# Optimization experiments

Hardware: AMD Instinct MI355X
Metric: run time of the kernel (lower is better)

Reference implementation:

```python
import jax, jax.numpy as jnp
import numpy as np

EPS = 1e-6
NH, HD = 8, 16            # num_heads, head_dim (dim=128)
KSS, DILS, HPR = (3, 5), (1, 2), (6, 2)  # kernel sizes, dilations, heads per range (favor_small)


def gelu(t):
    return jax.nn.gelu(t, approximate=False)


def conv1x1(x, w, b):
    # x: (B,C,H,W), w: (O,C), b: (O,)
    return jnp.einsum('oc,bchw->bohw', w, x) + b[None, :, None, None]


def dwconv(x, w, b, dil=1):
    # depthwise conv, w: (C,1,k,k)
    k = w.shape[-1]
    p = (k // 2) * dil
    y = jax.lax.conv_general_dilated(
        x, w, window_strides=(1, 1), padding=[(p, p), (p, p)],
        rhs_dilation=(dil, dil), feature_group_count=x.shape[1],
        dimension_numbers=('NCHW', 'OIHW', 'NCHW'))
    return y + b[None, :, None, None]


def ln2d(x, w, b):
    # LayerNorm over channel dim of NCHW
    mu = x.mean(axis=1, keepdims=True)
    var = ((x - mu) ** 2).mean(axis=1, keepdims=True)
    return (x - mu) * jax.lax.rsqrt(var + EPS) * w[None, :, None, None] + b[None, :, None, None]


def unfold(x, ks, dil):
    # x: (B,h,d,H,W) -> (B,h,d,L,H,W) with L=ks*ks neighborhood (row-major, matches F.unfold)
    B, h, d, H, W = x.shape
    p = (ks // 2) * dil
    xp = jnp.pad(x, ((0, 0), (0, 0), (0, 0), (p, p), (p, p)))
    patches = [xp[..., i * dil:i * dil + H, j * dil:j * dil + W]
               for i in range(ks) for j in range(ks)]
    return jnp.stack(patches, axis=3)


def neighborhood_attn(x, qkv_ws, qkv_bs, proj_w, proj_b):
    B, C, H, W = x.shape
    scale = HD ** -0.5
    outs, hs = [], 0
    for i in range(2):
        qkv = conv1x1(x, qkv_ws[i], qkv_bs[i]).reshape(B, 3, NH, HD, H, W)
        he = hs + HPR[i]
        q, k, v = qkv[:, 0, hs:he], qkv[:, 1, hs:he], qkv[:, 2, hs:he]
        k_nb = unfold(k, KSS[i], DILS[i])  # (B,h,d,L,H,W)
        v_nb = unfold(v, KSS[i], DILS[i])
        logits = jnp.einsum('bhdxy,bhdlxy->bhlxy', q * scale, k_nb)
        attn = jax.nn.softmax(logits, axis=2)
        outs.append(jnp.einsum('bhlxy,bhdlxy->bhdxy', attn, v_nb))
        hs = he
    out = jnp.concatenate(outs, axis=1).reshape(B, C, H, W)
    return conv1x1(out, proj_w, proj_b)


def msconvstar(x, fc1_w, fc1_b, dw_ws, dw_bs, fc2_w, fc2_b):
    h = conv1x1(x, fc1_w, fc1_b)                  # (B,192,H,W)
    xs = jnp.split(h, [64, 128], axis=1)          # channels [64,64,64] for dw_sizes (1,3,5)
    ys = [dwconv(t, w, b) for t, w, b in zip(xs, dw_ws, dw_bs)]
    h = h + jnp.concatenate(ys, axis=1)
    x1, x2 = jnp.split(h, 2, axis=1)
    return conv1x1(gelu(x1) * x2, fc2_w, fc2_b)


def cascaded_sparse(x, dw0_w, dw0_b, dw1_w, dw1_b, pw_w, pw_b):
    x = gelu(dwconv(x, dw0_w, dw0_b, dil=1))
    x = gelu(dwconv(x, dw1_w, dw1_b, dil=2))
    return conv1x1(x, pw_w, pw_b)


def setup_inputs() -> dict:
    key = jax.random.key(0)
    ks = jax.random.split(key, 24)
    C, HID = 128, 192

    def p(k, shape, s=0.02):
        return jax.random.normal(k, shape, jnp.float32) * s

    d = {'x': jax.random.normal(ks[0], (4, C, 80, 80), jnp.float32)}
    for i in (1, 2, 3, 4):
        d[f'n{i}_w'] = jnp.ones((C,), jnp.float32)
        d[f'n{i}_b'] = jnp.zeros((C,), jnp.float32)
    d['qkv0_w'] = p(ks[1], (3 * C, C)); d['qkv0_b'] = jnp.zeros((3 * C,), jnp.float32)
    d['qkv1_w'] = p(ks[2], (3 * C, C)); d['qkv1_b'] = jnp.zeros((3 * C,), jnp.float32)
    d['ma_proj_w'] = p(ks[3], (C, C)); d['ma_proj_b'] = jnp.zeros((C,), jnp.float32)
    for pre, k0 in (('m1', 4), ('m2', 10)):
        d[f'{pre}_fc1_w'] = p(ks[k0], (HID, C)); d[f'{pre}_fc1_b'] = jnp.zeros((HID,), jnp.float32)
        for j, dk in enumerate((1, 3, 5)):
            d[f'{pre}_dw{j}_w'] = p(ks[k0 + 1 + j], (64, 1, dk, dk))
            d[f'{pre}_dw{j}_b'] = jnp.zeros((64,), jnp.float32)
        d[f'{pre}_fc2_w'] = p(ks[k0 + 4], (C, HID // 2)); d[f'{pre}_fc2_b'] = jnp.zeros((C,), jnp.float32)
    d['sma_dw0_w'] = p(ks[16], (C, 1, 3, 3)); d['sma_dw0_b'] = jnp.zeros((C,), jnp.float32)
    d['sma_dw1_w'] = p(ks[17], (C, 1, 3, 3)); d['sma_dw1_b'] = jnp.zeros((C,), jnp.float32)
    d['sma_pw_w'] = p(ks[18], (C, C)); d['sma_pw_b'] = jnp.zeros((C,), jnp.float32)
    return d


def reference(x, n1_w, n1_b, n2_w, n2_b, n3_w, n3_b, n4_w, n4_b,
              qkv0_w, qkv0_b, qkv1_w, qkv1_b, ma_proj_w, ma_proj_b,
              m1_fc1_w, m1_fc1_b, m1_dw0_w, m1_dw0_b, m1_dw1_w, m1_dw1_b,
              m1_dw2_w, m1_dw2_b, m1_fc2_w, m1_fc2_b,
              sma_dw0_w, sma_dw0_b, sma_dw1_w, sma_dw1_b, sma_pw_w, sma_pw_b,
              m2_fc1_w, m2_fc1_b, m2_dw0_w, m2_dw0_b, m2_dw1_w, m2_dw1_b,
              m2_dw2_w, m2_dw2_b, m2_fc2_w, m2_fc2_b):
    x = x + neighborhood_attn(ln2d(x, n1_w, n1_b), (qkv0_w, qkv1_w), (qkv0_b, qkv1_b), ma_proj_w, ma_proj_b)
    x = x + msconvstar(ln2d(x, n2_w, n2_b), m1_fc1_w, m1_fc1_b,
                       (m1_dw0_w, m1_dw1_w, m1_dw2_w), (m1_dw0_b, m1_dw1_b, m1_dw2_b), m1_fc2_w, m1_fc2_b)
    x = x + cascaded_sparse(ln2d(x, n3_w, n3_b), sma_dw0_w, sma_dw0_b, sma_dw1_w, sma_dw1_b, sma_pw_w, sma_pw_b)
    x = x + msconvstar(ln2d(x, n4_w, n4_b), m2_fc1_w, m2_fc1_b,
                       (m2_dw0_w, m2_dw1_w, m2_dw2_w), (m2_dw0_b, m2_dw1_b, m2_dw2_b), m2_fc2_w, m2_fc2_b)
    return x
```

## Files before the change

kernel.cpp:

```cpp
#include <hip/hip_runtime.h>
#include <math.h>

#define Hn 80
#define Wn 80
#define HWn 6400

typedef unsigned short u16;
typedef __attribute__((ext_vector_type(8))) short s16x8;
typedef __attribute__((ext_vector_type(4))) float f32x4;

__device__ __forceinline__ float gelu_exact(float v) {
  return 0.5f * v * (1.f + erff(v * 0.70710678118654752f));
}
__device__ __forceinline__ u16 f2bf(float x) {
  unsigned u = __float_as_uint(x);
  return (u16)((u + 0x7fffu + ((u >> 16) & 1u)) >> 16);
}
typedef __attribute__((address_space(1))) const unsigned int* gptr_t;
typedef __attribute__((address_space(3))) unsigned int* lptr_t;
__device__ __forceinline__ void gld16(const void* g, void* l) {
  __builtin_amdgcn_global_load_lds((gptr_t)g, (lptr_t)l, 16, 0, 0);
}
__device__ __forceinline__ void ld16h(const u16* p, float* f) {
  uint4 a = *(const uint4*)p;
  uint4 c = *(const uint4*)(p + 8);
  unsigned w[8] = {a.x, a.y, a.z, a.w, c.x, c.y, c.z, c.w};
  #pragma unroll
  for (int j = 0; j < 8; ++j) {
    f[2 * j]     = __uint_as_float(w[j] << 16);
    f[2 * j + 1] = __uint_as_float(w[j] & 0xffff0000u);
  }
}

__global__ __launch_bounds__(256) void wprep_k(
    const float* __restrict__ q0w, const float* __restrict__ q0b,
    const float* __restrict__ q1w, const float* __restrict__ q1b,
    const float* __restrict__ projw, const float* __restrict__ f1w_1,
    const float* __restrict__ f2w_1, const float* __restrict__ pww,
    const float* __restrict__ f1w_2, const float* __restrict__ f2w_2,
    u16* Wq, float* Bq, u16* Wp, u16* Wf1a, u16* Wf2a, u16* Wpw, u16* Wf1b, u16* Wf2b) {
  int idx = blockIdx.x * 256 + threadIdx.x;
  if (idx < 49152) {
    int r = idx >> 7, ic = idx & 127;
    int sel = r >> 7, c = r & 127;
    const float* src = ((c >> 4) < 6 ? q0w : q1w);
    Wq[idx] = f2bf(src[(size_t)(sel * 128 + c) * 128 + ic]);
    return;
  }
  idx -= 49152;
  if (idx < 16384) { Wp[idx] = f2bf(projw[idx]); return; }
  idx -= 16384;
  if (idx < 24576) { Wf1a[idx] = f2bf(f1w_1[idx]); return; }
  idx -= 24576;
  if (idx < 16384) { int oc = idx >> 7, ic = idx & 127;
    Wf2a[idx] = ic < 96 ? f2bf(f2w_1[oc * 96 + ic]) : (u16)0; return; }
  idx -= 16384;
  if (idx < 16384) { Wpw[idx] = f2bf(pww[idx]); return; }
  idx -= 16384;
  if (idx < 24576) { Wf1b[idx] = f2bf(f1w_2[idx]); return; }
  idx -= 24576;
  if (idx < 16384) { int oc = idx >> 7, ic = idx & 127;
    Wf2b[idx] = ic < 96 ? f2bf(f2w_2[oc * 96 + ic]) : (u16)0; return; }
  idx -= 16384;
  if (idx < 384) {
    int sel = idx >> 7, c = idx & 127;
    Bq[idx] = ((c >> 4) < 6 ? q0b : q1b)[sel * 128 + c];
  }
}

template<int TMODE>
__global__ __launch_bounds__(256) void ln_k(const float* __restrict__ in,
    const float* __restrict__ gw, const float* __restrict__ gb, void* __restrict__ outv) {
  __shared__ float sS[4][64];
  __shared__ float sQ[4][64];
  __shared__ unsigned sT[64 * 64];
  const int b = blockIdx.y;
  const int p0 = blockIdx.x * 64;
  const int tid = threadIdx.x;
  const int px = tid & 63;
  const int cg = tid >> 6;
  const float* ip = in + (size_t)b * 128 * HWn + p0 + px;
  float s = 0.f, q = 0.f;
  #pragma unroll 8
  for (int c = cg * 32; c < cg * 32 + 32; ++c) { float v = ip[(size_t)c * HWn]; s += v; q += v * v; }
  sS[cg][px] = s; sQ[cg][px] = q;
  __syncthreads();
  float S = sS[0][px] + sS[1][px] + sS[2][px] + sS[3][px];
  float Q = sQ[0][px] + sQ[1][px] + sQ[2][px] + sQ[3][px];
  float mu = S * (1.f / 128.f);
  float rs = rsqrtf(Q * (1.f / 128.f) - mu * mu + 1e-6f);
  #pragma unroll
  for (int j = 0; j < 16; ++j) {
    int c0 = cg * 32 + 2 * j;
    float v0 = ip[(size_t)c0 * HWn];
    float v1 = ip[(size_t)(c0 + 1) * HWn];
    v0 = (v0 - mu) * rs * gw[c0] + gb[c0];
    v1 = (v1 - mu) * rs * gw[c0 + 1] + gb[c0 + 1];
    int wc = cg * 16 + j;
    sT[px * 64 + (wc ^ (px & 31))] = (unsigned)f2bf(v0) | ((unsigned)f2bf(v1) << 16);
  }
  __syncthreads();
  u16* ob = (u16*)outv + ((size_t)b * HWn + p0) * 128;
  #pragma unroll
  for (int it = 0; it < 4; ++it) {
    int opx = it * 16 + (tid >> 4);
    int chunk = tid & 15;
    unsigned w[4];
    #pragma unroll
    for (int j = 0; j < 4; ++j)
      w[j] = sT[opx * 64 + ((chunk * 4 + j) ^ (opx & 31))];
    *(uint4*)(ob + (size_t)opx * 128 + chunk * 8) = make_uint4(w[0], w[1], w[2], w[3]);
  }
}

__global__ __launch_bounds__(256) void lnstats_k(const float* __restrict__ in,
                                                 float2* __restrict__ st) {
  __shared__ float sS[4][64];
  __shared__ float sQ[4][64];
  const int b = blockIdx.y;
  const int p0 = blockIdx.x * 64;
  const int tid = threadIdx.x;
  const int px = tid & 63;
  const int cg = tid >> 6;
  const float* ip = in + (size_t)b * 128 * HWn + p0 + px;
  float s = 0.f, q = 0.f;
  #pragma unroll 8
  for (int c = cg * 32; c < cg * 32 + 32; ++c) { float v = ip[(size_t)c * HWn]; s += v; q += v * v; }
  sS[cg][px] = s; sQ[cg][px] = q;
  __syncthreads();
  if (cg == 0) {
    float S = sS[0][px] + sS[1][px] + sS[2][px] + sS[3][px];
    float Q = sQ[0][px] + sQ[1][px] + sQ[2][px] + sQ[3][px];
    float mu = S * (1.f / 128.f);
    float rs = rsqrtf(Q * (1.f / 128.f) - mu * mu + 1e-6f);
    st[(size_t)b * HWn + p0 + px] = make_float2(mu, rs);
  }
}

__device__ __forceinline__ s16x8 ldfrag(const u16* s, int row, int gk) {
  return *(const s16x8*)(s + row * 128 + ((gk ^ (row & 7)) << 3));
}

template<int ORIENT, int RES, int SPLITQ>
__global__ __launch_bounds__(256) void gemm_k(
    const u16* __restrict__ Xg, const u16* __restrict__ Wg,
    const float* __restrict__ bias, const float* __restrict__ resid,
    float* __restrict__ outF, u16* __restrict__ outH, int OCT) {
  __shared__ u16 sX[128 * 128];
  __shared__ u16 sW[64 * 128];
  const int tid = threadIdx.x, lane = tid & 63, wv = tid >> 6;
  const int b = blockIdx.y;
  const int px0 = blockIdx.x * 128;
  const int oc0 = blockIdx.z * 64;
  const u16* xb = Xg + ((size_t)b * HWn + px0) * 128;
  const u16* wb = Wg + (size_t)oc0 * 128;
  #pragma unroll
  for (int i = 0; i < 8; ++i) {
    int o16 = (wv * 8 + i) * 64 + lane;
    int r = o16 >> 4, g = o16 & 15;
    gld16(xb + (size_t)r * 128 + ((g ^ (r & 7)) << 3), (char*)sX + (size_t)(wv * 8 + i) * 1024);
  }
  #pragma unroll
  for (int i = 0; i < 4; ++i) {
    int o16 = (wv * 4 + i) * 64 + lane;
    int r = o16 >> 4, g = o16 & 15;
    gld16(wb + (size_t)r * 128 + ((g ^ (r & 7)) << 3), (char*)sW + (size_t)(wv * 4 + i) * 1024);
  }
  __syncthreads();
  const int l15 = lane & 15, l4 = lane >> 4;
  if (ORIENT == 0) {
    f32x4 acc[4][2] = {};
    #pragma unroll
    for (int ks = 0; ks < 4; ++ks) {
      int gk = ks * 4 + l4;
      s16x8 a[4], bb[2];
      #pragma unroll
      for (int mi = 0; mi < 4; ++mi) a[mi] = ldfrag(sW, mi * 16 + l15, gk);
      #pragma unroll
      for (int ni = 0; ni < 2; ++ni) bb[ni] = ldfrag(sX, wv * 32 + ni * 16 + l15, gk);
      #pragma unroll
      for (int mi = 0; mi < 4; ++mi)
        #pragma unroll
        for (int ni = 0; ni < 2; ++ni)
          acc[mi][ni] = __builtin_amdgcn_mfma_f32_16x16x32_bf16(a[mi], bb[ni], acc[mi][ni], 0, 0, 0);
    }
    #pragma unroll
    for (int mi = 0; mi < 4; ++mi) {
      #pragma unroll
      for (int rr = 0; rr < 4; ++rr) {
        int oc = oc0 + mi * 16 + l4 * 4 + rr;
        float bv = bias[oc];
        #pragma unroll
        for (int ni = 0; ni < 2; ++ni) {
          size_t idx = ((size_t)b * OCT + oc) * HWn + px0 + wv * 32 + ni * 16 + l15;
          float v = acc[mi][ni][rr] + bv;
          if (RES) v += resid[idx];
          outF[idx] = v;
        }
      }
    }
  } else {
    f32x4 acc[2][4] = {};
    #pragma unroll
    for (int ks = 0; ks < 4; ++ks) {
      int gk = ks * 4 + l4;
      s16x8 a[2], bb[4];
      #pragma unroll
      for (int mi = 0; mi < 2; ++mi) a[mi] = ldfrag(sX, wv * 32 + mi * 16 + l15, gk);
      #pragma unroll
      for (int ni = 0; ni < 4; ++ni) bb[ni] = ldfrag(sW, ni * 16 + l15, gk);
      #pragma unroll
      for (int mi = 0; mi < 2; ++mi)
        #pragma unroll
        for (int ni = 0; ni < 4; ++ni)
          acc[mi][ni] = __builtin_amdgcn_mfma_f32_16x16x32_bf16(a[mi], bb[ni], acc[mi][ni], 0, 0, 0);
    }
    #pragma unroll
    for (int ni = 0; ni < 4; ++ni) {
      int oc = oc0 + ni * 16 + l15;
      float bv = bias[oc];
      #pragma unroll
      for (int mi = 0; mi < 2; ++mi) {
        #pragma unroll
        for (int rr = 0; rr < 4; ++rr) {
          int px = px0 + wv * 32 + mi * 16 + l4 * 4 + rr;
          float v = acc[mi][ni][rr] + bv;
          u16 hv = f2bf(v);
          if (SPLITQ) {
            int sel = oc >> 7, c = oc & 127;
            int head = c >> 4, d = c & 15;
            outH[((((size_t)sel * 8 + head) * 4 + b) * HWn + px) * 16 + d] = hv;
          } else {
            outH[((size_t)b * HWn + px) * (size_t)OCT + oc] = hv;
          }
        }
      }
    }
  }
}

template<int KS, int DIL>
__device__ __forceinline__ void natt_body(const u16* __restrict__ qkv,
                                          u16* __restrict__ out, int b, int h, int p) {
  const int y = p / Wn, x = p - (p / Wn) * Wn;
  const u16* Qb = qkv + (((size_t)h * 4 + b) * HWn) * 16;
  const u16* Kb = qkv + ((((size_t)8 + h) * 4 + b) * HWn) * 16;
  const u16* Vb = qkv + ((((size_t)16 + h) * 4 + b) * HWn) * 16;
  float qv[16];
  ld16h(Qb + (size_t)p * 16, qv);
  #pragma unroll
  for (int d = 0; d < 16; ++d) qv[d] *= 0.25f;
  constexpr int L = KS * KS;
  float lg[L];
  #pragma unroll
  for (int i = 0; i < KS; ++i) {
    #pragma unroll
    for (int j = 0; j < KS; ++j) {
      int yy = y + (i - KS / 2) * DIL;
      int xx = x + (j - KS / 2) * DIL;
      float a = 0.f;
      if (yy >= 0 && yy < Hn && xx >= 0 && xx < Wn) {
        float kv[16];
        ld16h(Kb + (size_t)(yy * Wn + xx) * 16, kv);
        #pragma unroll
        for (int d = 0; d < 16; ++d) a = fmaf(qv[d], kv[d], a);
      }
      lg[i * KS + j] = a;
    }
  }
  float mx = lg[0];
  #pragma unroll
  for (int l = 1; l < L; ++l) mx = fmaxf(mx, lg[l]);
  float sum = 0.f;
  #pragma unroll
  for (int l = 0; l < L; ++l) { float e = __expf(lg[l] - mx); lg[l] = e; sum += e; }
  float inv = 1.f / sum;
  float acc[16];
  #pragma unroll
  for (int d = 0; d < 16; ++d) acc[d] = 0.f;
  #pragma unroll
  for (int i = 0; i < KS; ++i) {
    #pragma unroll
    for (int j = 0; j < KS; ++j) {
      int yy = y + (i - KS / 2) * DIL;
      int xx = x + (j - KS / 2) * DIL;
      if (yy >= 0 && yy < Hn && xx >= 0 && xx < Wn) {
        float vv[16];
        ld16h(Vb + (size_t)(yy * Wn + xx) * 16, vv);
        float wl = lg[i * KS + j] * inv;
        #pragma unroll
        for (int d = 0; d < 16; ++d) acc[d] = fmaf(wl, vv[d], acc[d]);
      }
    }
  }
  unsigned wst[8];
  #pragma unroll
  for (int j = 0; j < 8; ++j)
    wst[j] = (unsigned)f2bf(acc[2 * j]) | ((unsigned)f2bf(acc[2 * j + 1]) << 16);
  u16* op = out + ((size_t)b * HWn + p) * 128 + h * 16;
  *(uint4*)op = make_uint4(wst[0], wst[1], wst[2], wst[3]);
  *(uint4*)(op + 8) = make_uint4(wst[4], wst[5], wst[6], wst[7]);
}

__global__ __launch_bounds__(256) void natt_k(const u16* __restrict__ qkv,
                                              u16* __restrict__ out) {
  const int b = blockIdx.y, h = blockIdx.z;
  const int p = blockIdx.x * 256 + threadIdx.x;
  if (h < 6) natt_body<3, 1>(qkv, out, b, h, p);
  else       natt_body<5, 2>(qkv, out, b, h, p);
}

template<int R>
__device__ __forceinline__ void stage_plane(const float* __restrict__ plane,
                                            float* __restrict__ s,
                                            int ty0, int tx0, int tid) {
  constexpr int D = 16 + 2 * R, PD = D + 1;
  #pragma unroll
  for (int i = tid; i < D * D; i += 256) {
    int ey = i / D, ex = i - ey * D;
    int gy = ty0 - R + ey, gx = tx0 - R + ex;
    float v = 0.f;
    if (gy >= 0 && gy < Hn && gx >= 0 && gx < Wn) v = plane[gy * Wn + gx];
    s[ey * PD + ex] = v;
  }
}

template<int R>
__device__ __forceinline__ float dw_from_lds(const float* __restrict__ s, int ly, int lx,
                                             const float* __restrict__ w, float bv) {
  constexpr int PD = 16 + 2 * R + 1;
  float center = s[(ly + R) * PD + (lx + R)];
  float acc = bv;
  #pragma unroll
  for (int i = 0; i < 2 * R + 1; ++i)
    #pragma unroll
    for (int j = 0; j < 2 * R + 1; ++j)
      acc = fmaf(w[i * (2 * R + 1) + j], s[(ly + i) * PD + (lx + j)], acc);
  return center + acc;
}

template<int R1, int R2>
__device__ __forceinline__ void star_pairs(const float* __restrict__ hb,
    const float* __restrict__ w0, const float* __restrict__ b0,
    const float* __restrict__ w1, const float* __restrict__ b1,
    const float* __restrict__ w2, const float* __restrict__ b2,
    float* __restrict__ s1_0, float* __restrict__ s1_1,
    float* __restrict__ s2_0, float* __restrict__ s2_1,
    int z, int ty0, int tx0, int tid, int ly, int lx, unsigned* __restrict__ res) {
  if (R1 > 0) stage_plane<R1>(hb + (size_t)(z * 8) * HWn, s1_0, ty0, tx0, tid);
  stage_plane<R2>(hb + (size_t)(z * 8 + 96) * HWn, s2_0, ty0, tx0, tid);
  __syncthreads();
  #pragma unroll 1
  for (int pi = 0; pi < 8; ++pi) {
    int c1 = z * 8 + pi;
    int c2 = c1 + 96;
    float* s1c = (pi & 1) ? s1_1 : s1_0;
    float* s2c = (pi & 1) ? s2_1 : s2_0;
    if (pi < 7) {
      float* s1n = (pi & 1) ? s1_0 : s1_1;
      float* s2n = (pi & 1) ? s2_0 : s2_1;
      if (R1 > 0) stage_plane<R1>(hb + (size_t)(c1 + 1) * HWn, s1n, ty0, tx0, tid);
      stage_plane<R2>(hb + (size_t)(c2 + 1) * HWn, s2n, ty0, tx0, tid);
    }
    float h1;
    if constexpr (R1 == 0) {
      float cen = hb[(size_t)c1 * HWn + (ty0 + ly) * Wn + tx0 + lx];
      h1 = cen + fmaf(cen, w0[c1], b0[c1]);
    } else {
      h1 = dw_from_lds<R1>(s1c, ly, lx, w1 + (c1 - 64) * 9, b1[c1 - 64]);
    }
    float h2;
    if constexpr (R2 == 1) {
      h2 = dw_from_lds<1>(s2c, ly, lx, w1 + (c2 - 64) * 9, b1[c2 - 64]);
    } else {
      h2 = dw_from_lds<2>(s2c, ly, lx, w2 + (c2 - 128) * 25, b2[c2 - 128]);
    }
    u16 gv = f2bf(gelu_exact(h1) * h2);
    if (pi & 1) res[pi >> 1] |= ((unsigned)gv) << 16;
    else        res[pi >> 1] = (unsigned)gv;
    __syncthreads();
  }
}

__global__ __launch_bounds__(256) void star_k(const float* __restrict__ hbuf,
    const float* __restrict__ w0, const float* __restrict__ b0,
    const float* __restrict__ w1, const float* __restrict__ b1,
    const float* __restrict__ w2, const float* __restrict__ b2,
    u16* __restrict__ g) {
  __shared__ float s1_0[18 * 19];
  __shared__ float s1_1[18 * 19];
  __shared__ float s2_0[20 * 21];
  __shared__ float s2_1[20 * 21];
  const int b = blockIdx.y, z = blockIdx.z;
  const int tile = blockIdx.x;
  const int ty0 = (tile / 5) * 16, tx0 = (tile % 5) * 16;
  const int tid = threadIdx.x;
  const int ly = tid >> 4, lx = tid & 15;
  const float* hb = hbuf + (size_t)b * 192 * HWn;
  unsigned res[4];
  if (z < 4)      star_pairs<0, 1>(hb, w0, b0, w1, b1, w2, b2, s1_0, s1_1, s2_0, s2_1, z, ty0, tx0, tid, ly, lx, res);
  else if (z < 8) star_pairs<0, 2>(hb, w0, b0, w1, b1, w2, b2, s1_0, s1_1, s2_0, s2_1, z, ty0, tx0, tid, ly, lx, res);
  else            star_pairs<1, 2>(hb, w0, b0, w1, b1, w2, b2, s1_0, s1_1, s2_0, s2_1, z, ty0, tx0, tid, ly, lx, res);
  const int px = (ty0 + ly) * Wn + tx0 + lx;
  *(uint4*)(g + ((size_t)b * HWn + px) * 128 + z * 8) = make_uint4(res[0], res[1], res[2], res[3]);
  if (z < 4)
    *(uint4*)(g + ((size_t)b * HWn + px) * 128 + 96 + z * 8) = make_uint4(0, 0, 0, 0);
}

__global__ __launch_bounds__(256) void dwgf_k(const float* __restrict__ xin,
    const float2* __restrict__ st,
    const float* __restrict__ gw, const float* __restrict__ gb,
    const float* __restrict__ w1, const float* __restrict__ b1,
    const float* __restrict__ w2, const float* __restrict__ b2,
    u16* __restrict__ out) {
  __shared__ float sA[22 * 23];
  __shared__ float sB[20 * 21];
  __shared__ float sMu[22 * 22];
  __shared__ float sRs[22 * 22];
  const int b = blockIdx.y, z = blockIdx.z;
  const int tile = blockIdx.x;
  const int ty0 = (tile / 5) * 16, tx0 = (tile % 5) * 16;
  const int tid = threadIdx.x;
  const int ly = tid >> 4, lx = tid & 15;
  #pragma unroll
  for (int i = tid; i < 22 * 22; i += 256) {
    int ey = i / 22, ex = i - ey * 22;
    int gy = ty0 - 3 + ey, gx = tx0 - 3 + ex;
    float2 s = make_float2(0.f, 0.f);
    if (gy >= 0 && gy < Hn && gx >= 0 && gx < Wn) s = st[(size_t)b * HWn + gy * Wn + gx];
    sMu[i] = s.x; sRs[i] = s.y;
  }
  const float* xb = xin + (size_t)b * 128 * HWn;
  unsigned res[4];
  #pragma unroll 1
  for (int ci = 0; ci < 8; ++ci) {
    int c = z * 8 + ci;
    const float* xp = xb + (size_t)c * HWn;
    float gwc = gw[c], gbc = gb[c];
    __syncthreads();
    #pragma unroll
    for (int i = tid; i < 22 * 22; i += 256) {
      int ey = i / 22, ex = i - ey * 22;
      int gy = ty0 - 3 + ey, gx = tx0 - 3 + ex;
      float v = 0.f;
      if (gy >= 0 && gy < Hn && gx >= 0 && gx < Wn)
        v = (xp[gy * Wn + gx] - sMu[i]) * sRs[i] * gwc + gbc;
      sA[ey * 23 + ex] = v;
    }
    __syncthreads();
    #pragma unroll
    for (int j = tid; j < 20 * 20; j += 256) {
      int by = j / 20, bx = j - by * 20;
      int gy = ty0 - 2 + by, gx = tx0 - 2 + bx;
      float r = 0.f;
      if (gy >= 0 && gy < Hn && gx >= 0 && gx < Wn) {
        float acc = b1[c];
        #pragma unroll
        for (int di = 0; di < 3; ++di)
          #pragma unroll
          for (int dj = 0; dj < 3; ++dj)
            acc = fmaf(w1[c * 9 + di * 3 + dj], sA[(by + di) * 23 + (bx + dj)], acc);
        r = gelu_exact(acc);
      }
      sB[by * 21 + bx] = r;
    }
    __syncthreads();
    float acc = b2[c];
    #pragma unroll
    for (int di = 0; di < 3; ++di)
      #pragma unroll
      for (int dj = 0; dj < 3; ++dj)
        acc = fmaf(w2[c * 9 + di * 3 + dj], sB[(ly + 2 * di) * 21 + (lx + 2 * dj)], acc);
    float r = gelu_exact(acc);
    u16 gv = f2bf(r);
    if (ci & 1) res[ci >> 1] |= ((unsigned)gv) << 16;
    else        res[ci >> 1] = (unsigned)gv;
  }
  const int px = (ty0 + ly) * Wn + tx0 + lx;
  *(uint4*)(out + ((size_t)b * HWn + px) * 128 + z * 8) = make_uint4(res[0], res[1], res[2], res[3]);
}

extern "C" void kernel_launch(void* const* d_in, const int* in_sizes, int n_in,
                              void* d_out, int out_size, void* d_ws, size_t ws_size,
                              hipStream_t stream) {
  (void)in_sizes; (void)n_in; (void)out_size; (void)ws_size;
  const float* x      = (const float*)d_in[0];
  const float* n1w    = (const float*)d_in[1];
  const float* n1b    = (const float*)d_in[2];
  const float* n2w    = (const float*)d_in[3];
  const float* n2b    = (const float*)d_in[4];
  const float* n3w    = (const float*)d_in[5];
  const float* n3b    = (const float*)d_in[6];
  const float* n4w    = (const float*)d_in[7];
  const float* n4b    = (const float*)d_in[8];
  const float* qkv0w  = (const float*)d_in[9];
  const float* qkv0b  = (const float*)d_in[10];
  const float* qkv1w  = (const float*)d_in[11];
  const float* qkv1b  = (const float*)d_in[12];
  const float* projw  = (const float*)d_in[13];
  const float* projb  = (const float*)d_in[14];
  const float* m1fc1w = (const float*)d_in[15];
  const float* m1fc1b = (const float*)d_in[16];
  const float* m1dw0w = (const float*)d_in[17];
  const float* m1dw0b = (const float*)d_in[18];
  const float* m1dw1w = (const float*)d_in[19];
  const float* m1dw1b = (const float*)d_in[20];
  const float* m1dw2w = (const float*)d_in[21];
  const float* m1dw2b = (const float*)d_in[22];
  const float* m1fc2w = (const float*)d_in[23];
  const float* m1fc2b = (const float*)d_in[24];
  const float* smadw0w = (const float*)d_in[25];
  const float* smadw0b = (const float*)d_in[26];
  const float* smadw1w = (const float*)d_in[27];
  const float* smadw1b = (const float*)d_in[28];
  const float* smapww  = (const float*)d_in[29];
  const float* smapwb  = (const float*)d_in[30];
  const float* m2fc1w = (const float*)d_in[31];
  const float* m2fc1b = (const float*)d_in[32];
  const float* m2dw0w = (const float*)d_in[33];
  const float* m2dw0b = (const float*)d_in[34];
  const float* m2dw1w = (const float*)d_in[35];
  const float* m2dw1b = (const float*)d_in[36];
  const float* m2dw2w = (const float*)d_in[37];
  const float* m2dw2b = (const float*)d_in[38];
  const float* m2fc2w = (const float*)d_in[39];
  const float* m2fc2b = (const float*)d_in[40];

  float* out = (float*)d_out;
  char* wsb = (char*)d_ws;
  u16*  QKV = (u16*)(wsb + 0);
  float* Hb = (float*)(wsb + 0);
  u16*  LNo = (u16*)(wsb + 19660800);
  u16*  ATT = (u16*)(wsb + 26214400);
  u16*  T2  = (u16*)(wsb + 32768000);
  char* wp = wsb + 39321600;
  u16* Wq    = (u16*)wp;  wp += 98304;
  u16* Wproj = (u16*)wp;  wp += 32768;
  u16* Wf1a  = (u16*)wp;  wp += 49152;
  u16* Wf2a  = (u16*)wp;  wp += 32768;
  u16* Wpw   = (u16*)wp;  wp += 32768;
  u16* Wf1b  = (u16*)wp;  wp += 49152;
  u16* Wf2b  = (u16*)wp;  wp += 32768;
  float* Bq  = (float*)wp; wp += 2048;
  float2* Stats = (float2*)wp;

  dim3 blk(256);
  wprep_k<<<642, blk, 0, stream>>>(qkv0w, qkv0b, qkv1w, qkv1b, projw, m1fc1w, m1fc2w,
                                   smapww, m2fc1w, m2fc2w,
                                   Wq, Bq, Wproj, Wf1a, Wf2a, Wpw, Wf1b, Wf2b);

  ln_k<1><<<dim3(100, 4), blk, 0, stream>>>(x, n1w, n1b, LNo);
  gemm_k<1, 0, 1><<<dim3(50, 4, 6), blk, 0, stream>>>(LNo, Wq, Bq, nullptr, nullptr, QKV, 384);
  natt_k<<<dim3(25, 4, 8), blk, 0, stream>>>(QKV, ATT);
  gemm_k<0, 1, 0><<<dim3(50, 4, 2), blk, 0, stream>>>(ATT, Wproj, projb, x, out, nullptr, 128);

  ln_k<1><<<dim3(100, 4), blk, 0, stream>>>(out, n2w, n2b, LNo);
  gemm_k<0, 0, 0><<<dim3(50, 4, 3), blk, 0, stream>>>(LNo, Wf1a, m1fc1b, nullptr, Hb, nullptr, 192);
  star_k<<<dim3(25, 4, 12), blk, 0, stream>>>(Hb, m1dw0w, m1dw0b, m1dw1w, m1dw1b, m1dw2w, m1dw2b, ATT);
  gemm_k<0, 1, 0><<<dim3(50, 4, 2), blk, 0, stream>>>(ATT, Wf2a, m1fc2b, out, out, nullptr, 128);

  lnstats_k<<<dim3(100, 4), blk, 0, stream>>>(out, Stats);
  dwgf_k<<<dim3(25, 4, 16), blk, 0, stream>>>(out, Stats, n3w, n3b,
                                              smadw0w, smadw0b, smadw1w, smadw1b, T2);
  gemm_k<0, 1, 0><<<dim3(50, 4, 2), blk, 0, stream>>>(T2, Wpw, smapwb, out, out, nullptr, 128);

  ln_k<1><<<dim3(100, 4), blk, 0, stream>>>(out, n4w, n4b, LNo);
  gemm_k<0, 0, 0><<<dim3(50, 4, 3), blk, 0, stream>>>(LNo, Wf1b, m2fc1b, nullptr, Hb, nullptr, 192);
  star_k<<<dim3(25, 4, 12), blk, 0, stream>>>(Hb, m2dw0w, m2dw0b, m2dw1w, m2dw1b, m2dw2w, m2dw2b, ATT);
  gemm_k<0, 1, 0><<<dim3(50, 4, 2), blk, 0, stream>>>(ATT, Wf2b, m2fc2b, out, out, nullptr, 128);
}
```

Measured before the change: 169.0 us.

## Tile neighborhood attention with LDS halos and store fc1 output as bf16

The neighborhood attention kernel is split into two templated launches (3x3 dil1 and 5x5 dil2). Each block now stages a 16x16 tile of K and V plus its halo into shared memory, which removes per-neighbor bounds checks and redundant global loads. Separately, the fc1 GEMM writes its intermediate in bf16 instead of fp32, and the star depthwise kernel reads bf16. This halves that buffer's traffic but adds rounding to an intermediate that was previously kept in fp32.

```diff
diff --git a/kernel.cpp b/kernel.cpp
--- a/kernel.cpp
+++ b/kernel.cpp
@@ -15,6 +15,9 @@
 __device__ __forceinline__ u16 f2bf(float x) {
   unsigned u = __float_as_uint(x);
   return (u16)((u + 0x7fffu + ((u >> 16) & 1u)) >> 16);
+}
+__device__ __forceinline__ float bf2f(u16 h) {
+  return __uint_as_float(((unsigned)h) << 16);
 }
 typedef __attribute__((address_space(1))) const unsigned int* gptr_t;
 typedef __attribute__((address_space(3))) unsigned int* lptr_t;
@@ -68,9 +71,8 @@
   }
 }
 
-template<int TMODE>
 __global__ __launch_bounds__(256) void ln_k(const float* __restrict__ in,
-    const float* __restrict__ gw, const float* __restrict__ gb, void* __restrict__ outv) {
+    const float* __restrict__ gw, const float* __restrict__ gb, u16* __restrict__ outv) {
   __shared__ float sS[4][64];
   __shared__ float sQ[4][64];
   __shared__ unsigned sT[64 * 64];
@@ -100,7 +102,7 @@
     sT[px * 64 + (wc ^ (px & 31))] = (unsigned)f2bf(v0) | ((unsigned)f2bf(v1) << 16);
   }
   __syncthreads();
-  u16* ob = (u16*)outv + ((size_t)b * HWn + p0) * 128;
+  u16* ob = outv + ((size_t)b * HWn + p0) * 128;
   #pragma unroll
   for (int it = 0; it < 4; ++it) {
     int opx = it * 16 + (tid >> 4);
@@ -141,7 +143,7 @@
   return *(const s16x8*)(s + row * 128 + ((gk ^ (row & 7)) << 3));
 }
 
-template<int ORIENT, int RES, int SPLITQ>
+template<int ORIENT, int RES, int SPLITQ, int H16>
 __global__ __launch_bounds__(256) void gemm_k(
     const u16* __restrict__ Xg, const u16* __restrict__ Wg,
     const float* __restrict__ bias, const float* __restrict__ resid,
@@ -194,8 +196,12 @@
         for (int ni = 0; ni < 2; ++ni) {
           size_t idx = ((size_t)b * OCT + oc) * HWn + px0 + wv * 32 + ni * 16 + l15;
           float v = acc[mi][ni][rr] + bv;
-          if (RES) v += resid[idx];
-          outF[idx] = v;
+          if (H16) {
+            outH[idx] = f2bf(v);
+          } else {
+            if (RES) v += resid[idx];
+            outF[idx] = v;
+          }
         }
       }
     }
@@ -240,31 +246,50 @@
 }
 
 template<int KS, int DIL>
-__device__ __forceinline__ void natt_body(const u16* __restrict__ qkv,
-                                          u16* __restrict__ out, int b, int h, int p) {
-  const int y = p / Wn, x = p - (p / Wn) * Wn;
+__global__ __launch_bounds__(256) void natt_k(const u16* __restrict__ qkv,
+                                              u16* __restrict__ out, int h0) {
+  constexpr int HALO = DIL * (KS / 2);
+  constexpr int D = 16 + 2 * HALO;
+  __shared__ u16 sK[D * D * 16];
+  __shared__ u16 sV[D * D * 16];
+  const int b = blockIdx.y, h = h0 + blockIdx.z;
+  const int tile = blockIdx.x;
+  const int ty0 = (tile / 5) * 16, tx0 = (tile % 5) * 16;
+  const int tid = threadIdx.x;
+  const int ly = tid >> 4, lx = tid & 15;
   const u16* Qb = qkv + (((size_t)h * 4 + b) * HWn) * 16;
   const u16* Kb = qkv + ((((size_t)8 + h) * 4 + b) * HWn) * 16;
   const u16* Vb = qkv + ((((size_t)16 + h) * 4 + b) * HWn) * 16;
+  for (int i = tid; i < D * D * 2; i += 256) {
+    int pxi = i >> 1, half = i & 1;
+    int ey = pxi / D, ex = pxi - ey * D;
+    int gy = ty0 - HALO + ey, gx = tx0 - HALO + ex;
+    uint4 kv = make_uint4(0, 0, 0, 0), vv = make_uint4(0, 0, 0, 0);
+    if (gy >= 0 && gy < Hn && gx >= 0 && gx < Wn) {
+      size_t off = (size_t)(gy * Wn + gx) * 16 + half * 8;
+      kv = *(const uint4*)(Kb + off);
+      vv = *(const uint4*)(Vb + off);
+    }
+    *(uint4*)(sK + pxi * 16 + half * 8) = kv;
+    *(uint4*)(sV + pxi * 16 + half * 8) = vv;
+  }
+  const int p = (ty0 + ly) * Wn + tx0 + lx;
   float qv[16];
   ld16h(Qb + (size_t)p * 16, qv);
   #pragma unroll
   for (int d = 0; d < 16; ++d) qv[d] *= 0.25f;
+  __syncthreads();
   constexpr int L = KS * KS;
   float lg[L];
   #pragma unroll
   for (int i = 0; i < KS; ++i) {
     #pragma unroll
     for (int j = 0; j < KS; ++j) {
-      int yy = y + (i - KS / 2) * DIL;
-      int xx = x + (j - KS / 2) * DIL;
+      float kvv[16];
+      ld16h(sK + (size_t)((ly + i * DIL) * D + lx + j * DIL) * 16, kvv);
       float a = 0.f;
-      if (yy >= 0 && yy < Hn && xx >= 0 && xx < Wn) {
-        float kv[16];
-        ld16h(Kb + (size_t)(yy * Wn + xx) * 16, kv);
-        #pragma unroll
-        for (int d = 0; d < 16; ++d) a = fmaf(qv[d], kv[d], a);
-      }
+      #pragma unroll
+      for (int d = 0; d < 16; ++d) a = fmaf(qv[d], kvv[d], a);
       lg[i * KS + j] = a;
     }
   }
@@ -282,15 +307,11 @@
   for (int i = 0; i < KS; ++i) {
     #pragma unroll
     for (int j = 0; j < KS; ++j) {
-      int yy = y + (i - KS / 2) * DIL;
-      int xx = x + (j - KS / 2) * DIL;
-      if (yy >= 0 && yy < Hn && xx >= 0 && xx < Wn) {
-        float vv[16];
-        ld16h(Vb + (size_t)(yy * Wn + xx) * 16, vv);
-        float wl = lg[i * KS + j] * inv;
-        #pragma unroll
-        for (int d = 0; d < 16; ++d) acc[d] = fmaf(wl, vv[d], acc[d]);
-      }
+      float vv[16];
+      ld16h(sV + (size_t)((ly + i * DIL) * D + lx + j * DIL) * 16, vv);
+      float wl = lg[i * KS + j] * inv;
+      #pragma unroll
+      for (int d = 0; d < 16; ++d) acc[d] = fmaf(wl, vv[d], acc[d]);
     }
   }
   unsigned wst[8];
@@ -302,16 +323,8 @@
   *(uint4*)(op + 8) = make_uint4(wst[4], wst[5], wst[6], wst[7]);
 }
 
-__global__ __launch_bounds__(256) void natt_k(const u16* __restrict__ qkv,
-                                              u16* __restrict__ out) {
-  const int b = blockIdx.y, h = blockIdx.z;
-  const int p = blockIdx.x * 256 + threadIdx.x;
-  if (h < 6) natt_body<3, 1>(qkv, out, b, h, p);
-  else       natt_body<5, 2>(qkv, out, b, h, p);
-}
-
 template<int R>
-__device__ __forceinline__ void stage_plane(const float* __restrict__ plane,
+__device__ __forceinline__ void stage_plane(const u16* __restrict__ plane,
                                             float* __restrict__ s,
                                             int ty0, int tx0, int tid) {
   constexpr int D = 16 + 2 * R, PD = D + 1;
@@ -320,7 +333,7 @@
     int ey = i / D, ex = i - ey * D;
     int gy = ty0 - R + ey, gx = tx0 - R + ex;
     float v = 0.f;
-    if (gy >= 0 && gy < Hn && gx >= 0 && gx < Wn) v = plane[gy * Wn + gx];
+    if (gy >= 0 && gy < Hn && gx >= 0 && gx < Wn) v = bf2f(plane[gy * Wn + gx]);
     s[ey * PD + ex] = v;
   }
 }
@@ -340,7 +353,7 @@
 }
 
 template<int R1, int R2>
-__device__ __forceinline__ void star_pairs(const float* __restrict__ hb,
+__device__ __forceinline__ void star_pairs(const u16* __restrict__ hb,
     const float* __restrict__ w0, const float* __restrict__ b0,
     const float* __restrict__ w1, const float* __restrict__ b1,
     const float* __restrict__ w2, const float* __restrict__ b2,
@@ -364,7 +377,7 @@
     }
     float h1;
     if constexpr (R1 == 0) {
-      float cen = hb[(size_t)c1 * HWn + (ty0 + ly) * Wn + tx0 + lx];
+      float cen = bf2f(hb[(size_t)c1 * HWn + (ty0 + ly) * Wn + tx0 + lx]);
       h1 = cen + fmaf(cen, w0[c1], b0[c1]);
     } else {
       h1 = dw_from_lds<R1>(s1c, ly, lx, w1 + (c1 - 64) * 9, b1[c1 - 64]);
@@ -382,7 +395,7 @@
   }
 }
 
-__global__ __launch_bounds__(256) void star_k(const float* __restrict__ hbuf,
+__global__ __launch_bounds__(256) void star_k(const u16* __restrict__ hbuf,
     const float* __restrict__ w0, const float* __restrict__ b0,
     const float* __restrict__ w1, const float* __restrict__ b1,
     const float* __restrict__ w2, const float* __restrict__ b2,
@@ -396,7 +409,7 @@
   const int ty0 = (tile / 5) * 16, tx0 = (tile % 5) * 16;
   const int tid = threadIdx.x;
   const int ly = tid >> 4, lx = tid & 15;
-  const float* hb = hbuf + (size_t)b * 192 * HWn;
+  const u16* hb = hbuf + (size_t)b * 192 * HWn;
   unsigned res[4];
   if (z < 4)      star_pairs<0, 1>(hb, w0, b0, w1, b1, w2, b2, s1_0, s1_1, s2_0, s2_1, z, ty0, tx0, tid, ly, lx, res);
   else if (z < 8) star_pairs<0, 2>(hb, w0, b0, w1, b1, w2, b2, s1_0, s1_1, s2_0, s2_1, z, ty0, tx0, tid, ly, lx, res);
@@ -529,7 +542,7 @@
   float* out = (float*)d_out;
   char* wsb = (char*)d_ws;
   u16*  QKV = (u16*)(wsb + 0);
-  float* Hb = (float*)(wsb + 0);
+  u16*  Hb16 = (u16*)(wsb + 0);
   u16*  LNo = (u16*)(wsb + 19660800);
   u16*  ATT = (u16*)(wsb + 26214400);
   u16*  T2  = (u16*)(wsb + 32768000);
@@ -549,23 +562,24 @@
                                    smapww, m2fc1w, m2fc2w,
                                    Wq, Bq, Wproj, Wf1a, Wf2a, Wpw, Wf1b, Wf2b);
 
-  ln_k<1><<<dim3(100, 4), blk, 0, stream>>>(x, n1w, n1b, LNo);
-  gemm_k<1, 0, 1><<<dim3(50, 4, 6), blk, 0, stream>>>(LNo, Wq, Bq, nullptr, nullptr, QKV, 384);
-  natt_k<<<dim3(25, 4, 8), blk, 0, stream>>>(QKV, ATT);
-  gemm_k<0, 1, 0><<<dim3(50, 4, 2), blk, 0, stream>>>(ATT, Wproj, projb, x, out, nullptr, 128);
-
-  ln_k<1><<<dim3(100, 4), blk, 0, stream>>>(out, n2w, n2b, LNo);
-  gemm_k<0, 0, 0><<<dim3(50, 4, 3), blk, 0, stream>>>(LNo, Wf1a, m1fc1b, nullptr, Hb, nullptr, 192);
-  star_k<<<dim3(25, 4, 12), blk, 0, stream>>>(Hb, m1dw0w, m1dw0b, m1dw1w, m1dw1b, m1dw2w, m1dw2b, ATT);
-  gemm_k<0, 1, 0><<<dim3(50, 4, 2), blk, 0, stream>>>(ATT, Wf2a, m1fc2b, out, out, nullptr, 128);
+  ln_k<<<dim3(100, 4), blk, 0, stream>>>(x, n1w, n1b, LNo);
+  gemm_k<1, 0, 1, 0><<<dim3(50, 4, 6), blk, 0, stream>>>(LNo, Wq, Bq, nullptr, nullptr, QKV, 384);
+  natt_k<3, 1><<<dim3(25, 4, 6), blk, 0, stream>>>(QKV, ATT, 0);
+  natt_k<5, 2><<<dim3(25, 4, 2), blk, 0, stream>>>(QKV, ATT, 6);
+  gemm_k<0, 1, 0, 0><<<dim3(50, 4, 2), blk, 0, stream>>>(ATT, Wproj, projb, x, out, nullptr, 128);
+
+  ln_k<<<dim3(100, 4), blk, 0, stream>>>(out, n2w, n2b, LNo);
+  gemm_k<0, 0, 0, 1><<<dim3(50, 4, 3), blk, 0, stream>>>(LNo, Wf1a, m1fc1b, nullptr, nullptr, Hb16, 192);
+  star_k<<<dim3(25, 4, 12), blk, 0, stream>>>(Hb16, m1dw0w, m1dw0b, m1dw1w, m1dw1b, m1dw2w, m1dw2b, ATT);
+  gemm_k<0, 1, 0, 0><<<dim3(50, 4, 2), blk, 0, stream>>>(ATT, Wf2a, m1fc2b, out, out, nullptr, 128);
 
   lnstats_k<<<dim3(100, 4), blk, 0, stream>>>(out, Stats);
   dwgf_k<<<dim3(25, 4, 16), blk, 0, stream>>>(out, Stats, n3w, n3b,
                                               smadw0w, smadw0b, smadw1w, smadw1b, T2);
-  gemm_k<0, 1, 0><<<dim3(50, 4, 2), blk, 0, stream>>>(T2, Wpw, smapwb, out, out, nullptr, 128);
-
-  ln_k<1><<<dim3(100, 4), blk, 0, stream>>>(out, n4w, n4b, LNo);
-  gemm_k<0, 0, 0><<<dim3(50, 4, 3), blk, 0, stream>>>(LNo, Wf1b, m2fc1b, nullptr, Hb, nullptr, 192);
-  star_k<<<dim3(25, 4, 12), blk, 0, stream>>>(Hb, m2dw0w, m2dw0b, m2dw1w, m2dw1b, m2dw2w, m2dw2b, ATT);
-  gemm_k<0, 1, 0><<<dim3(50, 4, 2), blk, 0, stream>>>(ATT, Wf2b, m2fc2b, out, out, nullptr, 128);
-}
+  gemm_k<0, 1, 0, 0><<<dim3(50, 4, 2), blk, 0, stream>>>(T2, Wpw, smapwb, out, out, nullptr, 128);
+
+  ln_k<<<dim3(100, 4), blk, 0, stream>>>(out, n4w, n4b, LNo);
+  gemm_k<0, 0, 0, 1><<<dim3(50, 4, 3), blk, 0, stream>>>(LNo, Wf1b, m2fc1b, nullptr, nullptr, Hb16, 192);
+  star_k<<<dim3(25, 4, 12), blk, 0, stream>>>(Hb16, m2dw0w, m2dw0b, m2dw1w, m2dw1b, m2dw2w, m2dw2b, ATT);
+  gemm_k<0, 1, 0, 0><<<dim3(50, 4, 2), blk, 0, stream>>>(ATT, Wf2b, m2fc2b, out, out, nullptr, 128);
+}
```

Result: faster. 163.9 us (-3.0%).
